# Kernel tuning notes

Measured on AMD Instinct MI355X. Metric: run time of the kernel, lower is better.

## Reference

```python
import jax, jax.numpy as jnp
import numpy as np

N = 100000   # nodes
E = 1200000  # directed edges (avg degree 12)
D = 64       # in_feats
C = 40       # n_classes
K = 16       # propagation steps
ALPHA = 0.05


def setup_inputs() -> dict:
    key = jax.random.key(0)
    k1, k2, k3, k4 = jax.random.split(key, 4)
    feat = jax.random.normal(k1, (N, D), jnp.float32)
    # xavier_uniform for fc.weight [C, D]
    limit = np.sqrt(6.0 / (D + C)).astype(np.float32)
    W = jax.random.uniform(k2, (C, D), jnp.float32, -limit, limit)
    b = jnp.zeros((C,), jnp.float32)
    src = jax.random.randint(k3, (E,), 0, N, dtype=jnp.int32)
    dst = jax.random.randint(k4, (E,), 0, N, dtype=jnp.int32)
    return {"feat": feat, "W": W, "b": b, "src": src, "dst": dst}


def reference(feat, W, b, src, dst):
    # --- getNormAugAdj: A_hat = D^{-1/2} (A + I) D^{-1/2} ---
    loops = jnp.arange(N, dtype=src.dtype)
    row = jnp.concatenate([dst, loops])  # output node of each edge
    col = jnp.concatenate([src, loops])  # input  node of each edge
    ones = jnp.ones(row.shape, feat.dtype)
    deg = jax.ops.segment_sum(ones, row, num_segments=N)  # >= 1 (self-loops)
    dinv = jax.lax.rsqrt(deg)
    w = dinv[row] * dinv[col]  # per-edge normalized weight

    def spmm(x):  # x: [N, D] -> A_hat @ x
        return jax.ops.segment_sum(w[:, None] * x[col], row, num_segments=N)

    feat_ori = feat

    # SSGC loop (faithful to the original, including h /= K inside the loop)
    def step(carry, _):
        x, h = carry
        x = spmm(x)
        h = (h + (1.0 - ALPHA) * x + ALPHA * feat_ori) / K
        return (x, h), None

    (_, h), _ = jax.lax.scan(step, (feat, jnp.zeros_like(feat)), None, length=K)

    # fc(h)
    return h @ W.T + b
```

## Files before the change

### kernel.cpp

```cpp
#include <hip/hip_runtime.h>
#include <hip/hip_fp16.h>

#define NN 100000
#define EE 1200000
#define DD 64
#define CC 40
#define KK 16
#define BSZ 196
#define NBK 512
#define TCAP 3072
#define EPB 4096
#define ABLK ((EE + EPB - 1) / EPB)
#define PL1 (NN * 4)
#define GBLK ((NN + 11) / 12)

struct __align__(8) ERec { int c; float w; };

__global__ __launch_bounds__(512) void curinit_kernel(int* __restrict__ cursor) {
    int b = threadIdx.x;
    if (b < NBK) cursor[b] = b * TCAP;
}

__global__ __launch_bounds__(256) void sortA_kernel(const int* __restrict__ src,
                                                    const int* __restrict__ dst,
                                                    int* __restrict__ cursor,
                                                    int2* __restrict__ tmp) {
    __shared__ int2 stg[EPB];
    __shared__ int hist[NBK], loff[NBK], lcur[NBK], gbase[NBK];
    int t = threadIdx.x;
    long e0 = (long)blockIdx.x * EPB;
    int n = (int)((EE - e0 < EPB) ? (EE - e0) : EPB);
    for (int j = t; j < NBK; j += 256) hist[j] = 0;
    __syncthreads();
    int d[16], sx[16];
#pragma unroll
    for (int j = 0; j < 16; ++j) {
        int i = t + j * 256;
        if (i < n) {
            d[j] = dst[e0 + i];
            sx[j] = src[e0 + i];
            atomicAdd(&hist[d[j] / BSZ], 1);
        } else d[j] = -1;
    }
    __syncthreads();
    int c0 = hist[2 * t], c1 = hist[2 * t + 1];
    int s2 = c0 + c1;
    __syncthreads();
    loff[t] = s2;
    __syncthreads();
    for (int off = 1; off < 256; off <<= 1) {
        int u = (t >= off) ? loff[t - off] : 0;
        __syncthreads();
        loff[t] += u;
        __syncthreads();
    }
    int excl = loff[t] - s2;
    __syncthreads();
    loff[2 * t] = excl;          loff[2 * t + 1] = excl + c0;
    lcur[2 * t] = excl;          lcur[2 * t + 1] = excl + c0;
    gbase[2 * t]     = atomicAdd(&cursor[2 * t], c0);
    gbase[2 * t + 1] = atomicAdd(&cursor[2 * t + 1], c1);
    __syncthreads();
#pragma unroll
    for (int j = 0; j < 16; ++j) {
        if (d[j] >= 0) {
            int b = d[j] / BSZ;
            int p = atomicAdd(&lcur[b], 1);
            stg[p] = make_int2(d[j], sx[j]);
        }
    }
    __syncthreads();
    for (int i = t; i < n; i += 256) {
        int2 r = stg[i];
        int b = r.x / BSZ;
        int pos = gbase[b] + (i - loff[b]);
        if (pos < (b + 1) * TCAP) tmp[pos] = r;
    }
}

__global__ __launch_bounds__(512) void bscan_kernel(const int* __restrict__ cursor,
                                                    int* __restrict__ bbase,
                                                    int* __restrict__ row_ptr) {
    __shared__ int sm[512];
    int t = threadIdx.x;
    int v = (t < NBK) ? (cursor[t] - t * TCAP) : 0;
    sm[t] = v;
    __syncthreads();
    for (int off = 1; off < 512; off <<= 1) {
        int u = (t >= off) ? sm[t - off] : 0;
        __syncthreads();
        sm[t] += u;
        __syncthreads();
    }
    if (t < NBK) bbase[t] = sm[t] - v;
    if (t == 511) row_ptr[NN] = sm[511];
}

__global__ __launch_bounds__(256) void sortB_kernel(const int2* __restrict__ tmp,
                                                    const int* __restrict__ cursor,
                                                    const int* __restrict__ bbase,
                                                    float* __restrict__ dinv,
                                                    int* __restrict__ row_ptr,
                                                    int2* __restrict__ er2) {
    __shared__ int2 se[TCAP];
    __shared__ int2 so[TCAP];
    __shared__ int hist[256], lcur[256];
    int b = blockIdx.x;
    int n0 = b * BSZ;
    if (n0 >= NN) return;
    int n1 = n0 + BSZ; if (n1 > NN) n1 = NN;
    int nb = n1 - n0;
    int t = threadIdx.x;
    int cnt = cursor[b] - b * TCAP;
    int base = bbase[b];
    hist[t] = 0;
    __syncthreads();
    for (int i = t; i < cnt; i += 256) {
        int2 r = tmp[b * TCAP + i];
        se[i] = r;
        atomicAdd(&hist[r.x - n0], 1);
    }
    __syncthreads();
    if (t < nb) dinv[n0 + t] = rsqrtf((float)(hist[t] + 1));
    int v = hist[t];
    lcur[t] = v;
    __syncthreads();
    for (int off = 1; off < 256; off <<= 1) {
        int u = (t >= off) ? lcur[t - off] : 0;
        __syncthreads();
        lcur[t] += u;
        __syncthreads();
    }
    int excl = lcur[t] - v;
    __syncthreads();
    lcur[t] = excl;
    if (t < nb) row_ptr[n0 + t] = base + excl;
    __syncthreads();
    for (int i = t; i < cnt; i += 256) {
        int2 r = se[i];
        int ln = r.x - n0;
        int pos = atomicAdd(&lcur[ln], 1);
        so[pos] = make_int2(r.y, r.x);
    }
    __syncthreads();
    for (int i = t; i < cnt; i += 256) er2[base + i] = so[i];
}

__global__ __launch_bounds__(256) void wfill_kernel(const int2* __restrict__ er2,
                                                    const float* __restrict__ dinv,
                                                    int2* __restrict__ er) {
    int i = blockIdx.x * 256 + threadIdx.x;
    if (i >= EE) return;
    int2 r = er2[i];
    float w = dinv[r.y] * dinv[r.x];
    er[i] = make_int2(r.x, __float_as_int(w));
}

__global__ __launch_bounds__(256) void proj_kernel(const float4* __restrict__ feat4,
                                                   const float* __restrict__ W,
                                                   float4* __restrict__ y0) {
    __shared__ float smW[CC * 68];
    __shared__ float smF[64 * 68];
    __shared__ float smO[64 * 42];
    int t = threadIdx.x;
    for (int j = t; j < CC * 16; j += 256) {
        int c = j >> 4, q = j & 15;
        *(float4*)(smW + c * 68 + q * 4) = ((const float4*)W)[j];
    }
    int n0 = blockIdx.x * 64;
    for (int j = t; j < 64 * 16; j += 256) {
        int r = j >> 4, q = j & 15;
        if (n0 + r < NN)
            *(float4*)(smF + r * 68 + q * 4) = feat4[(size_t)(n0 + r) * 16 + q];
    }
    __syncthreads();
    int ln = t >> 2, c0 = (t & 3) * 10;
    int node = n0 + ln;
    float acc[10];
#pragma unroll
    for (int c = 0; c < 10; ++c) acc[c] = 0.f;
    if (node < NN) {
#pragma unroll
        for (int db = 0; db < 16; ++db) {
            float4 fv = *(const float4*)(smF + ln * 68 + db * 4);
#pragma unroll
            for (int c = 0; c < 10; ++c) {
                float4 wv = *(const float4*)(smW + (c0 + c) * 68 + db * 4);
                acc[c] = fmaf(fv.x, wv.x, acc[c]);
                acc[c] = fmaf(fv.y, wv.y, acc[c]);
                acc[c] = fmaf(fv.z, wv.z, acc[c]);
                acc[c] = fmaf(fv.w, wv.w, acc[c]);
            }
        }
    }
#pragma unroll
    for (int c = 0; c < 10; ++c) smO[ln * 42 + c0 + c] = acc[c];
    __syncthreads();
    for (int j = t; j < 64 * 5; j += 256) {
        int r = j / 5, q = j - r * 5;
        if (n0 + r < NN) {
            const float* s = smO + r * 42 + q * 8;
            float4 ov;
            __half2* op = (__half2*)&ov;
            op[0] = __floats2half2_rn(s[0], s[1]);
            op[1] = __floats2half2_rn(s[2], s[3]);
            op[2] = __floats2half2_rn(s[4], s[5]);
            op[3] = __floats2half2_rn(s[6], s[7]);
            y0[(q < 4) ? ((size_t)(n0 + r) * 4 + q) : (size_t)(PL1 + n0 + r)] = ov;
        }
    }
}

#define DEC8(V, F0, F1, F2, F3)                                             \
    const __half2* hp_##F0 = (const __half2*)&(V);                          \
    float2 F0 = __half22float2(hp_##F0[0]), F1 = __half22float2(hp_##F0[1]);\
    float2 F2 = __half22float2(hp_##F0[2]), F3 = __half22float2(hp_##F0[3]);

#define ACC8(R, V)                                                          \
    {                                                                       \
        DEC8(V, f0, f1, f2, f3)                                             \
        a0 = fmaf((R).w, f0.x, a0); a1 = fmaf((R).w, f0.y, a1);             \
        a2 = fmaf((R).w, f1.x, a2); a3 = fmaf((R).w, f1.y, a3);             \
        a4 = fmaf((R).w, f2.x, a4); a5 = fmaf((R).w, f2.y, a5);             \
        a6 = fmaf((R).w, f3.x, a6); a7 = fmaf((R).w, f3.y, a7);             \
    }

#define EDGE_LOOP                                                           \
    int e = beg;                                                            \
    int e8 = beg + ((end - beg) & ~7);                                      \
    for (; e < e8; e += 8) {                                                \
        ERec r0 = er[e], r1 = er[e + 1], r2 = er[e + 2], r3 = er[e + 3];    \
        ERec r4 = er[e + 4], r5 = er[e + 5], r6 = er[e + 6], r7 = er[e + 7];\
        float4 v0 = x[r0.c * m + a];                                        \
        float4 v1 = x[r1.c * m + a];                                        \
        float4 v2 = x[r2.c * m + a];                                        \
        float4 v3 = x[r3.c * m + a];                                        \
        float4 v4 = x[r4.c * m + a];                                        \
        float4 v5 = x[r5.c * m + a];                                        \
        float4 v6 = x[r6.c * m + a];                                        \
        float4 v7 = x[r7.c * m + a];                                        \
        ACC8(r0, v0); ACC8(r1, v1); ACC8(r2, v2); ACC8(r3, v3);             \
        ACC8(r4, v4); ACC8(r5, v5); ACC8(r6, v6); ACC8(r7, v7);             \
    }                                                                       \
    int e4 = e + ((end - e) & ~3);                                          \
    for (; e < e4; e += 4) {                                                \
        ERec r0 = er[e], r1 = er[e + 1], r2 = er[e + 2], r3 = er[e + 3];    \
        float4 v0 = x[r0.c * m + a];                                        \
        float4 v1 = x[r1.c * m + a];                                        \
        float4 v2 = x[r2.c * m + a];                                        \
        float4 v3 = x[r3.c * m + a];                                        \
        ACC8(r0, v0); ACC8(r1, v1); ACC8(r2, v2); ACC8(r3, v3);             \
    }                                                                       \
    for (; e < end; ++e) {                                                  \
        ERec r = er[e];                                                     \
        float4 v = x[r.c * m + a];                                          \
        ACC8(r, v);                                                         \
    }

__global__ __launch_bounds__(64) void spmm_prop(
    const float4* __restrict__ x, float4* __restrict__ x_out,
    const int* __restrict__ row_ptr, const ERec* __restrict__ er,
    const float* __restrict__ dinv) {
    int lane = threadIdx.x;
    int nw = lane / 5;
    int li = lane - nw * 5;
    int g = blockIdx.x * 12 + nw;
    if (nw >= 12 || g >= NN) return;
    int beg = row_ptr[g], end = row_ptr[g + 1];
    float di = dinv[g];
    float w0 = di * di;
    int m = (li < 4) ? 4 : 1;
    int a = (li < 4) ? li : PL1;
    int base = g * m + a;
    float4 sv = x[base];
    float a0, a1, a2, a3, a4, a5, a6, a7;
    {
        DEC8(sv, f0, f1, f2, f3)
        a0 = w0 * f0.x; a1 = w0 * f0.y; a2 = w0 * f1.x; a3 = w0 * f1.y;
        a4 = w0 * f2.x; a5 = w0 * f2.y; a6 = w0 * f3.x; a7 = w0 * f3.y;
    }
    EDGE_LOOP
    float4 ov;
    __half2* op = (__half2*)&ov;
    op[0] = __floats2half2_rn(a0, a1);
    op[1] = __floats2half2_rn(a2, a3);
    op[2] = __floats2half2_rn(a4, a5);
    op[3] = __floats2half2_rn(a6, a7);
    x_out[base] = ov;
}

__global__ __launch_bounds__(64) void spmm_final(
    const float4* __restrict__ x,
    const float4* __restrict__ x13p,
    const float4* __restrict__ x14p,
    const float4* __restrict__ y0,
    const float* __restrict__ bias,
    const int* __restrict__ row_ptr, const ERec* __restrict__ er,
    const float* __restrict__ dinv, float* __restrict__ outp) {
    int lane = threadIdx.x;
    int nw = lane / 5;
    int li = lane - nw * 5;
    int g = blockIdx.x * 12 + nw;
    if (nw >= 12 || g >= NN) return;
    int beg = row_ptr[g], end = row_ptr[g + 1];
    float di = dinv[g];
    float w0 = di * di;
    int m = (li < 4) ? 4 : 1;
    int a = (li < 4) ? li : PL1;
    int base = g * m + a;
    float4 sv = x[base];
    float s0, s1, s2, s3, s4, s5, s6, s7;
    float a0, a1, a2, a3, a4, a5, a6, a7;
    {
        DEC8(sv, f0, f1, f2, f3)
        s0 = f0.x; s1 = f0.y; s2 = f1.x; s3 = f1.y;
        s4 = f2.x; s5 = f2.y; s6 = f3.x; s7 = f3.y;
        a0 = w0 * s0; a1 = w0 * s1; a2 = w0 * s2; a3 = w0 * s3;
        a4 = w0 * s4; a5 = w0 * s5; a6 = w0 * s6; a7 = w0 * s7;
    }
    EDGE_LOOP
    const float C16 = 0.95f / 16.0f;
    const float C15 = 0.95f / 256.0f;
    const float C14 = 0.95f / 4096.0f;
    const float C13 = 0.95f / 65536.0f;
    const float FC  = 0.05f / 15.0f;
    float o0 = C16 * a0 + C15 * s0, o1 = C16 * a1 + C15 * s1;
    float o2 = C16 * a2 + C15 * s2, o3 = C16 * a3 + C15 * s3;
    float o4 = C16 * a4 + C15 * s4, o5 = C16 * a5 + C15 * s5;
    float o6 = C16 * a6 + C15 * s6, o7 = C16 * a7 + C15 * s7;
#define ADD8(P, CF)                                                         \
    {                                                                       \
        float4 v = (P)[base];                                               \
        DEC8(v, f0, f1, f2, f3)                                             \
        o0 = fmaf((CF), f0.x, o0); o1 = fmaf((CF), f0.y, o1);               \
        o2 = fmaf((CF), f1.x, o2); o3 = fmaf((CF), f1.y, o3);               \
        o4 = fmaf((CF), f2.x, o4); o5 = fmaf((CF), f2.y, o5);               \
        o6 = fmaf((CF), f3.x, o6); o7 = fmaf((CF), f3.y, o7);               \
    }
    ADD8(x14p, C14)
    ADD8(x13p, C13)
    ADD8(y0, FC)
#undef ADD8
    const float4* b4 = (const float4*)(bias + li * 8);
    float4 bb0 = b4[0], bb1 = b4[1];
    float4 w0v = make_float4(o0 + bb0.x, o1 + bb0.y, o2 + bb0.z, o3 + bb0.w);
    float4 w1v = make_float4(o4 + bb1.x, o5 + bb1.y, o6 + bb1.z, o7 + bb1.w);
    float4* op = (float4*)(outp + (size_t)g * CC + li * 8);
    op[0] = w0v; op[1] = w1v;
}

extern "C" void kernel_launch(void* const* d_in, const int* in_sizes, int n_in,
                              void* d_out, int out_size, void* d_ws, size_t ws_size,
                              hipStream_t stream) {
    const float* feat = (const float*)d_in[0];
    const float* W    = (const float*)d_in[1];
    const float* b    = (const float*)d_in[2];
    const int*   src  = (const int*)d_in[3];
    const int*   dst  = (const int*)d_in[4];
    float* out = (float*)d_out;

    char* p = (char*)d_ws;
    auto alloc = [&](size_t bytes) {
        char* r = p;
        p += (bytes + 255) & ~(size_t)255;
        return r;
    };
    float*   dinv    = (float*)alloc((size_t)NN * sizeof(float));
    int*     row_ptr = (int*)alloc((size_t)(NN + 1) * sizeof(int));
    int*     cursor  = (int*)alloc((size_t)NBK * sizeof(int));
    int*     bbase   = (int*)alloc((size_t)NBK * sizeof(int));
    int2*    tmp     = (int2*)alloc((size_t)NBK * TCAP * sizeof(int2));
    int2*    er2     = (int2*)alloc((size_t)EE * sizeof(int2));
    int2*    er      = (int2*)alloc((size_t)EE * sizeof(int2));
    float4*  y0      = (float4*)alloc((size_t)NN * 5 * sizeof(float4));
    float4*  xa      = (float4*)alloc((size_t)NN * 5 * sizeof(float4));
    float4*  xb      = (float4*)alloc((size_t)NN * 5 * sizeof(float4));
    float4*  x13b    = (float4*)alloc((size_t)NN * 5 * sizeof(float4));
    float4*  x14b    = (float4*)alloc((size_t)NN * 5 * sizeof(float4));
    float4*  x15b    = (float4*)alloc((size_t)NN * 5 * sizeof(float4));

    curinit_kernel<<<1, 512, 0, stream>>>(cursor);
    sortA_kernel<<<ABLK, 256, 0, stream>>>(src, dst, cursor, tmp);
    bscan_kernel<<<1, 512, 0, stream>>>(cursor, bbase, row_ptr);
    sortB_kernel<<<NBK, 256, 0, stream>>>(tmp, cursor, bbase, dinv, row_ptr, er2);
    wfill_kernel<<<(EE + 255) / 256, 256, 0, stream>>>(er2, dinv, er);
    proj_kernel<<<(NN + 63) / 64, 256, 0, stream>>>((const float4*)feat, W, y0);

    const float4* xs = y0;
    for (int j = 0; j < 12; ++j) {
        float4* xd = (j & 1) ? xb : xa;
        spmm_prop<<<GBLK, 64, 0, stream>>>(xs, xd, row_ptr, (const ERec*)er, dinv);
        xs = xd;
    }
    spmm_prop<<<GBLK, 64, 0, stream>>>(xs, x13b, row_ptr, (const ERec*)er, dinv);
    spmm_prop<<<GBLK, 64, 0, stream>>>(x13b, x14b, row_ptr, (const ERec*)er, dinv);
    spmm_prop<<<GBLK, 64, 0, stream>>>(x14b, x15b, row_ptr, (const ERec*)er, dinv);
    spmm_final<<<GBLK, 64, 0, stream>>>(x15b, x13b, x14b, y0, b, row_ptr,
                                        (const ERec*)er, dinv, out);
}
```

Measured before the change: 582.2 us.

## Pack edge records to 32 bits and split SpMM into three column-phase planes

Edge records drop from 8 bytes to 4 bytes by packing a 17-bit column index with a 15-bit fp16 weight, with the sign bit dropped since weights are positive. This halves edge-stream traffic, and those loads and the output stores become nontemporal. The feature layout is split into three planes (16+16+8 classes), each handled by a separate blockIdx.y phase. Each plane's gather touches a smaller contiguous footprint, aimed at better cache locality. The cost is that every edge list is read three times instead of once, and the weight loses precision to fp16.

Result: slower. 767.1 us (+31.8%).

```diff
diff --git a/kernel.cpp b/kernel.cpp
--- a/kernel.cpp
+++ b/kernel.cpp
@@ -11,8 +11,11 @@
 #define TCAP 3072
 #define EPB 4096
 #define ABLK ((EE + EPB - 1) / EPB)
-#define PL1 (NN * 4)
-#define GBLK ((NN + 11) / 12)
+#define GBLK32 ((NN + 31) / 32)
+#define P1OFF (NN * 2)
+#define P2OFF (NN * 4)
+
+typedef float vf4 __attribute__((ext_vector_type(4)));
 
 struct __align__(8) ERec { int c; float w; };
 
@@ -148,12 +151,13 @@
 
 __global__ __launch_bounds__(256) void wfill_kernel(const int2* __restrict__ er2,
                                                     const float* __restrict__ dinv,
-                                                    int2* __restrict__ er) {
+                                                    unsigned int* __restrict__ er4) {
     int i = blockIdx.x * 256 + threadIdx.x;
     if (i >= EE) return;
     int2 r = er2[i];
     float w = dinv[r.y] * dinv[r.x];
-    er[i] = make_int2(r.x, __float_as_int(w));
+    unsigned short hb = __half_as_ushort(__float2half_rn(w)) & 0x7FFF;
+    er4[i] = (unsigned int)r.x | ((unsigned int)hb << 17);
 }
 
 __global__ __launch_bounds__(256) void proj_kernel(const float4* __restrict__ feat4,
@@ -198,7 +202,8 @@
     __syncthreads();
     for (int j = t; j < 64 * 5; j += 256) {
         int r = j / 5, q = j - r * 5;
-        if (n0 + r < NN) {
+        int i = n0 + r;
+        if (i < NN) {
             const float* s = smO + r * 42 + q * 8;
             float4 ov;
             __half2* op = (__half2*)&ov;
@@ -206,7 +211,10 @@
             op[1] = __floats2half2_rn(s[2], s[3]);
             op[2] = __floats2half2_rn(s[4], s[5]);
             op[3] = __floats2half2_rn(s[6], s[7]);
-            y0[(q < 4) ? ((size_t)(n0 + r) * 4 + q) : (size_t)(PL1 + n0 + r)] = ov;
+            size_t idx = (q < 2) ? ((size_t)i * 2 + q)
+                       : (q < 4) ? ((size_t)P1OFF + i * 2 + (q - 2))
+                                 : ((size_t)P2OFF + i);
+            y0[idx] = ov;
         }
     }
 }
@@ -216,63 +224,88 @@
     float2 F0 = __half22float2(hp_##F0[0]), F1 = __half22float2(hp_##F0[1]);\
     float2 F2 = __half22float2(hp_##F0[2]), F3 = __half22float2(hp_##F0[3]);
 
-#define ACC8(R, V)                                                          \
+#define ACC8(WW, V)                                                         \
     {                                                                       \
         DEC8(V, f0, f1, f2, f3)                                             \
-        a0 = fmaf((R).w, f0.x, a0); a1 = fmaf((R).w, f0.y, a1);             \
-        a2 = fmaf((R).w, f1.x, a2); a3 = fmaf((R).w, f1.y, a3);             \
-        a4 = fmaf((R).w, f2.x, a4); a5 = fmaf((R).w, f2.y, a5);             \
-        a6 = fmaf((R).w, f3.x, a6); a7 = fmaf((R).w, f3.y, a7);             \
-    }
+        a0 = fmaf((WW), f0.x, a0); a1 = fmaf((WW), f0.y, a1);               \
+        a2 = fmaf((WW), f1.x, a2); a3 = fmaf((WW), f1.y, a3);               \
+        a4 = fmaf((WW), f2.x, a4); a5 = fmaf((WW), f2.y, a5);               \
+        a6 = fmaf((WW), f3.x, a6); a7 = fmaf((WW), f3.y, a7);               \
+    }
+
+#define WDEC(Q) __half2float(__ushort_as_half((unsigned short)((Q) >> 17)))
 
 #define EDGE_LOOP                                                           \
     int e = beg;                                                            \
     int e8 = beg + ((end - beg) & ~7);                                      \
     for (; e < e8; e += 8) {                                                \
-        ERec r0 = er[e], r1 = er[e + 1], r2 = er[e + 2], r3 = er[e + 3];    \
-        ERec r4 = er[e + 4], r5 = er[e + 5], r6 = er[e + 6], r7 = er[e + 7];\
-        float4 v0 = x[r0.c * m + a];                                        \
-        float4 v1 = x[r1.c * m + a];                                        \
-        float4 v2 = x[r2.c * m + a];                                        \
-        float4 v3 = x[r3.c * m + a];                                        \
-        float4 v4 = x[r4.c * m + a];                                        \
-        float4 v5 = x[r5.c * m + a];                                        \
-        float4 v6 = x[r6.c * m + a];                                        \
-        float4 v7 = x[r7.c * m + a];                                        \
-        ACC8(r0, v0); ACC8(r1, v1); ACC8(r2, v2); ACC8(r3, v3);             \
-        ACC8(r4, v4); ACC8(r5, v5); ACC8(r6, v6); ACC8(r7, v7);             \
+        unsigned q0 = __builtin_nontemporal_load(er + e);                   \
+        unsigned q1 = __builtin_nontemporal_load(er + e + 1);               \
+        unsigned q2 = __builtin_nontemporal_load(er + e + 2);               \
+        unsigned q3 = __builtin_nontemporal_load(er + e + 3);               \
+        unsigned q4 = __builtin_nontemporal_load(er + e + 4);               \
+        unsigned q5 = __builtin_nontemporal_load(er + e + 5);               \
+        unsigned q6 = __builtin_nontemporal_load(er + e + 6);               \
+        unsigned q7 = __builtin_nontemporal_load(er + e + 7);               \
+        float4 v0 = xp[(q0 & 0x1FFFFu) * st + li];                          \
+        float4 v1 = xp[(q1 & 0x1FFFFu) * st + li];                          \
+        float4 v2 = xp[(q2 & 0x1FFFFu) * st + li];                          \
+        float4 v3 = xp[(q3 & 0x1FFFFu) * st + li];                          \
+        float4 v4 = xp[(q4 & 0x1FFFFu) * st + li];                          \
+        float4 v5 = xp[(q5 & 0x1FFFFu) * st + li];                          \
+        float4 v6 = xp[(q6 & 0x1FFFFu) * st + li];                          \
+        float4 v7 = xp[(q7 & 0x1FFFFu) * st + li];                          \
+        ACC8(WDEC(q0), v0); ACC8(WDEC(q1), v1);                             \
+        ACC8(WDEC(q2), v2); ACC8(WDEC(q3), v3);                             \
+        ACC8(WDEC(q4), v4); ACC8(WDEC(q5), v5);                             \
+        ACC8(WDEC(q6), v6); ACC8(WDEC(q7), v7);                             \
     }                                                                       \
     int e4 = e + ((end - e) & ~3);                                          \
     for (; e < e4; e += 4) {                                                \
-        ERec r0 = er[e], r1 = er[e + 1], r2 = er[e + 2], r3 = er[e + 3];    \
-        float4 v0 = x[r0.c * m + a];                                        \
-        float4 v1 = x[r1.c * m + a];                                        \
-        float4 v2 = x[r2.c * m + a];                                        \
-        float4 v3 = x[r3.c * m + a];                                        \
-        ACC8(r0, v0); ACC8(r1, v1); ACC8(r2, v2); ACC8(r3, v3);             \
+        unsigned q0 = __builtin_nontemporal_load(er + e);                   \
+        unsigned q1 = __builtin_nontemporal_load(er + e + 1);               \
+        unsigned q2 = __builtin_nontemporal_load(er + e + 2);               \
+        unsigned q3 = __builtin_nontemporal_load(er + e + 3);               \
+        float4 v0 = xp[(q0 & 0x1FFFFu) * st + li];                          \
+        float4 v1 = xp[(q1 & 0x1FFFFu) * st + li];                          \
+        float4 v2 = xp[(q2 & 0x1FFFFu) * st + li];                          \
+        float4 v3 = xp[(q3 & 0x1FFFFu) * st + li];                          \
+        ACC8(WDEC(q0), v0); ACC8(WDEC(q1), v1);                             \
+        ACC8(WDEC(q2), v2); ACC8(WDEC(q3), v3);                             \
     }                                                                       \
     for (; e < end; ++e) {                                                  \
-        ERec r = er[e];                                                     \
-        float4 v = x[r.c * m + a];                                          \
-        ACC8(r, v);                                                         \
-    }
+        unsigned q = __builtin_nontemporal_load(er + e);                    \
+        float4 v = xp[(q & 0x1FFFFu) * st + li];                            \
+        ACC8(WDEC(q), v);                                                   \
+    }
+
+#define PHASE_SETUP(XBUF)                                                   \
+    int ph = blockIdx.y;                                                    \
+    int lane = threadIdx.x;                                                 \
+    int g, li, st;                                                          \
+    const float4* xp;                                                       \
+    if (ph < 2) {                                                           \
+        g = blockIdx.x * 32 + (lane >> 1);                                  \
+        li = lane & 1; st = 2;                                              \
+        xp = (XBUF) + (ph ? P1OFF : 0);                                     \
+    } else {                                                                \
+        if (lane >= 32) return;                                             \
+        g = blockIdx.x * 32 + lane;                                         \
+        li = 0; st = 1;                                                     \
+        xp = (XBUF) + P2OFF;                                                \
+    }                                                                       \
+    if (g >= NN) return;
 
 __global__ __launch_bounds__(64) void spmm_prop(
     const float4* __restrict__ x, float4* __restrict__ x_out,
-    const int* __restrict__ row_ptr, const ERec* __restrict__ er,
+    const int* __restrict__ row_ptr, const unsigned int* __restrict__ er,
     const float* __restrict__ dinv) {
-    int lane = threadIdx.x;
-    int nw = lane / 5;
-    int li = lane - nw * 5;
-    int g = blockIdx.x * 12 + nw;
-    if (nw >= 12 || g >= NN) return;
+    PHASE_SETUP(x)
     int beg = row_ptr[g], end = row_ptr[g + 1];
     float di = dinv[g];
     float w0 = di * di;
-    int m = (li < 4) ? 4 : 1;
-    int a = (li < 4) ? li : PL1;
-    int base = g * m + a;
-    float4 sv = x[base];
+    int base = g * st + li;
+    float4 sv = xp[base];
     float a0, a1, a2, a3, a4, a5, a6, a7;
     {
         DEC8(sv, f0, f1, f2, f3)
@@ -286,7 +319,8 @@
     op[1] = __floats2half2_rn(a2, a3);
     op[2] = __floats2half2_rn(a4, a5);
     op[3] = __floats2half2_rn(a6, a7);
-    x_out[base] = ov;
+    float4* dst4 = x_out + (xp - x) + base;
+    __builtin_nontemporal_store(*(const vf4*)&ov, (vf4*)dst4);
 }
 
 __global__ __launch_bounds__(64) void spmm_final(
@@ -295,20 +329,15 @@
     const float4* __restrict__ x14p,
     const float4* __restrict__ y0,
     const float* __restrict__ bias,
-    const int* __restrict__ row_ptr, const ERec* __restrict__ er,
+    const int* __restrict__ row_ptr, const unsigned int* __restrict__ er,
     const float* __restrict__ dinv, float* __restrict__ outp) {
-    int lane = threadIdx.x;
-    int nw = lane / 5;
-    int li = lane - nw * 5;
-    int g = blockIdx.x * 12 + nw;
-    if (nw >= 12 || g >= NN) return;
+    PHASE_SETUP(x)
     int beg = row_ptr[g], end = row_ptr[g + 1];
     float di = dinv[g];
     float w0 = di * di;
-    int m = (li < 4) ? 4 : 1;
-    int a = (li < 4) ? li : PL1;
-    int base = g * m + a;
-    float4 sv = x[base];
+    int base = g * st + li;
+    long poff = xp - x;
+    float4 sv = xp[base];
     float s0, s1, s2, s3, s4, s5, s6, s7;
     float a0, a1, a2, a3, a4, a5, a6, a7;
     {
@@ -330,7 +359,7 @@
     float o6 = C16 * a6 + C15 * s6, o7 = C16 * a7 + C15 * s7;
 #define ADD8(P, CF)                                                         \
     {                                                                       \
-        float4 v = (P)[base];                                               \
+        float4 v = (P)[poff + base];                                        \
         DEC8(v, f0, f1, f2, f3)                                             \
         o0 = fmaf((CF), f0.x, o0); o1 = fmaf((CF), f0.y, o1);               \
         o2 = fmaf((CF), f1.x, o2); o3 = fmaf((CF), f1.y, o3);               \
@@ -341,11 +370,12 @@
     ADD8(x13p, C13)
     ADD8(y0, FC)
 #undef ADD8
-    const float4* b4 = (const float4*)(bias + li * 8);
+    int d0 = (ph < 2) ? (ph * 16 + li * 8) : 32;
+    const float4* b4 = (const float4*)(bias + d0);
     float4 bb0 = b4[0], bb1 = b4[1];
     float4 w0v = make_float4(o0 + bb0.x, o1 + bb0.y, o2 + bb0.z, o3 + bb0.w);
     float4 w1v = make_float4(o4 + bb1.x, o5 + bb1.y, o6 + bb1.z, o7 + bb1.w);
-    float4* op = (float4*)(outp + (size_t)g * CC + li * 8);
+    float4* op = (float4*)(outp + (size_t)g * CC + d0);
     op[0] = w0v; op[1] = w1v;
 }
 
@@ -365,36 +395,37 @@
         p += (bytes + 255) & ~(size_t)255;
         return r;
     };
-    float*   dinv    = (float*)alloc((size_t)NN * sizeof(float));
-    int*     row_ptr = (int*)alloc((size_t)(NN + 1) * sizeof(int));
-    int*     cursor  = (int*)alloc((size_t)NBK * sizeof(int));
-    int*     bbase   = (int*)alloc((size_t)NBK * sizeof(int));
-    int2*    tmp     = (int2*)alloc((size_t)NBK * TCAP * sizeof(int2));
-    int2*    er2     = (int2*)alloc((size_t)EE * sizeof(int2));
-    int2*    er      = (int2*)alloc((size_t)EE * sizeof(int2));
-    float4*  y0      = (float4*)alloc((size_t)NN * 5 * sizeof(float4));
-    float4*  xa      = (float4*)alloc((size_t)NN * 5 * sizeof(float4));
-    float4*  xb      = (float4*)alloc((size_t)NN * 5 * sizeof(float4));
-    float4*  x13b    = (float4*)alloc((size_t)NN * 5 * sizeof(float4));
-    float4*  x14b    = (float4*)alloc((size_t)NN * 5 * sizeof(float4));
-    float4*  x15b    = (float4*)alloc((size_t)NN * 5 * sizeof(float4));
+    float*        dinv    = (float*)alloc((size_t)NN * sizeof(float));
+    int*          row_ptr = (int*)alloc((size_t)(NN + 1) * sizeof(int));
+    int*          cursor  = (int*)alloc((size_t)NBK * sizeof(int));
+    int*          bbase   = (int*)alloc((size_t)NBK * sizeof(int));
+    int2*         tmp     = (int2*)alloc((size_t)NBK * TCAP * sizeof(int2));
+    int2*         er2     = (int2*)alloc((size_t)EE * sizeof(int2));
+    unsigned int* er4     = (unsigned int*)alloc((size_t)EE * sizeof(int));
+    float4*       y0      = (float4*)alloc((size_t)NN * 5 * sizeof(float4));
+    float4*       xa      = (float4*)alloc((size_t)NN * 5 * sizeof(float4));
+    float4*       xb      = (float4*)alloc((size_t)NN * 5 * sizeof(float4));
+    float4*       x13b    = (float4*)alloc((size_t)NN * 5 * sizeof(float4));
+    float4*       x14b    = (float4*)alloc((size_t)NN * 5 * sizeof(float4));
+    float4*       x15b    = (float4*)alloc((size_t)NN * 5 * sizeof(float4));
 
     curinit_kernel<<<1, 512, 0, stream>>>(cursor);
     sortA_kernel<<<ABLK, 256, 0, stream>>>(src, dst, cursor, tmp);
     bscan_kernel<<<1, 512, 0, stream>>>(cursor, bbase, row_ptr);
     sortB_kernel<<<NBK, 256, 0, stream>>>(tmp, cursor, bbase, dinv, row_ptr, er2);
-    wfill_kernel<<<(EE + 255) / 256, 256, 0, stream>>>(er2, dinv, er);
+    wfill_kernel<<<(EE + 255) / 256, 256, 0, stream>>>(er2, dinv, er4);
     proj_kernel<<<(NN + 63) / 64, 256, 0, stream>>>((const float4*)feat, W, y0);
 
+    dim3 sgrid(GBLK32, 3);
     const float4* xs = y0;
     for (int j = 0; j < 12; ++j) {
         float4* xd = (j & 1) ? xb : xa;
-        spmm_prop<<<GBLK, 64, 0, stream>>>(xs, xd, row_ptr, (const ERec*)er, dinv);
+        spmm_prop<<<sgrid, 64, 0, stream>>>(xs, xd, row_ptr, er4, dinv);
         xs = xd;
     }
-    spmm_prop<<<GBLK, 64, 0, stream>>>(xs, x13b, row_ptr, (const ERec*)er, dinv);
-    spmm_prop<<<GBLK, 64, 0, stream>>>(x13b, x14b, row_ptr, (const ERec*)er, dinv);
-    spmm_prop<<<GBLK, 64, 0, stream>>>(x14b, x15b, row_ptr, (const ERec*)er, dinv);
-    spmm_final<<<GBLK, 64, 0, stream>>>(x15b, x13b, x14b, y0, b, row_ptr,
-                                        (const ERec*)er, dinv, out);
-}
+    spmm_prop<<<sgrid, 64, 0, stream>>>(xs, x13b, row_ptr, er4, dinv);
+    spmm_prop<<<sgrid, 64, 0, stream>>>(x13b, x14b, row_ptr, er4, dinv);
+    spmm_prop<<<sgrid, 64, 0, stream>>>(x14b, x15b, row_ptr, er4, dinv);
+    spmm_final<<<sgrid, 64, 0, stream>>>(x15b, x13b, x14b, y0, b, row_ptr,
+                                         er4, dinv, out);
+}
```
